# Optimization experiments

Hardware: AMD Instinct MI355X
Metric: run time of the kernel (lower is better)

## Reference

```python
import jax, jax.numpy as jnp
import numpy as np

INV_SCALE = 16.0  # 2 ** 4
DROPOUT_P = 0.2


def setup_inputs() -> dict:
    key = jax.random.key(0)
    ks = jax.random.split(key, 8)
    Nq, Nk, D = 8192, 8192, 32
    return {
        "x1": jax.random.normal(ks[0], (Nq, D), jnp.float32),
        "x2": jax.random.normal(ks[1], (Nk, D), jnp.float32),
        "wq_w": jax.random.normal(ks[2], (4, D), jnp.float32) * 0.1,
        "wq_b": jax.random.normal(ks[3], (4,), jnp.float32) * 0.1,
        "wk_w": jax.random.normal(ks[4], (4, D), jnp.float32) * 0.1,
        "wk_b": jax.random.normal(ks[5], (4,), jnp.float32) * 0.1,
        "wv_w": jax.random.normal(ks[6], (8, D), jnp.float32) * 0.1,
        "wv_b": jax.random.normal(ks[7], (8,), jnp.float32) * 0.1,
    }


def reference(x1, x2, wq_w, wq_b, wk_w, wk_b, wv_w, wv_b):
    # Linear projections (torch Linear: x @ W.T + b)
    q = x1 @ wq_w.T + wq_b          # [Nq, 4]
    k = x2 @ wk_w.T + wk_b          # [Nk, 4]
    v = x2 @ wv_w.T + wv_b          # [Nk, 8]
    scores = (q @ k.T) / INV_SCALE  # [Nq, Nk]
    probs = jax.nn.softmax(scores, axis=-1)
    # Inverted dropout with a fixed key (deterministic reference)
    keep = jax.random.bernoulli(jax.random.key(42), 1.0 - DROPOUT_P, probs.shape)
    dropped = jnp.where(keep, probs / (1.0 - DROPOUT_P), 0.0)
    return dropped @ v              # [Nq, 8]
```

## Files before the change

kernel.cpp:

```cpp
#include <hip/hip_runtime.h>
#include <stdint.h>

#define NQ 8192
#define NK 8192
#define DIN 32

#define BT 256
#define RPW 4
#define ROWS_PER_BLOCK 16
#define CHUNK 512

#define KEEP_BITS 3435974144u
#define QSCALE 0.0901684060119172f

__device__ __forceinline__ uint32_t rotl(uint32_t v, int d) {
    return __builtin_amdgcn_alignbit(v, v, 32 - d);
}

__device__ __forceinline__ void round4(uint32_t x0[4], uint32_t x1[4], int d) {
#pragma unroll
    for (int j = 0; j < 4; ++j) {
        x0[j] += x1[j];
        x1[j] = rotl(x1[j], d);
        x1[j] ^= x0[j];
    }
}

__device__ __forceinline__ void inject4(uint32_t x0[4], uint32_t x1[4],
                                        uint32_t c0, uint32_t c1) {
#pragma unroll
    for (int j = 0; j < 4; ++j) { x0[j] += c0; x1[j] += c1; }
}

__device__ __forceinline__ void threefry4(uint32_t idx0, uint32_t bits[4]) {
    const uint32_t ks1 = 42u;
    const uint32_t ks2 = 0x1BD11BDAu ^ 42u;
    uint32_t x0[4], x1[4];
#pragma unroll
    for (int j = 0; j < 4; ++j) {
        x0[j] = 0u;
        x1[j] = idx0 + (uint32_t)j * (uint32_t)NK + ks1;
    }
    round4(x0, x1, 13); round4(x0, x1, 15); round4(x0, x1, 26); round4(x0, x1, 6);
    inject4(x0, x1, ks1, ks2 + 1u);
    round4(x0, x1, 17); round4(x0, x1, 29); round4(x0, x1, 16); round4(x0, x1, 24);
    inject4(x0, x1, ks2, 0u + 2u);
    round4(x0, x1, 13); round4(x0, x1, 15); round4(x0, x1, 26); round4(x0, x1, 6);
    inject4(x0, x1, 0u, ks1 + 3u);
    round4(x0, x1, 17); round4(x0, x1, 29); round4(x0, x1, 16); round4(x0, x1, 24);
    inject4(x0, x1, ks1, ks2 + 4u);
    round4(x0, x1, 13); round4(x0, x1, 15); round4(x0, x1, 26); round4(x0, x1, 6);
#pragma unroll
    for (int j = 0; j < 4; ++j) bits[j] = (x0[j] + ks2) ^ (x1[j] + 0u + 5u);
}

__device__ __forceinline__ float fexp2(float x) {
#if __has_builtin(__builtin_amdgcn_exp2f)
    return __builtin_amdgcn_exp2f(x);
#else
    return __expf(0.6931471805599453f * x);
#endif
}

__global__ void proj_kernel(const float* __restrict__ x,
                            const float* __restrict__ w,
                            const float* __restrict__ b,
                            float* __restrict__ out, int dout) {
    __shared__ __align__(16) float ws[8 * DIN];
    __shared__ float bs[8];
    const int tid = threadIdx.x;
    if (tid < dout * DIN) ws[tid] = w[tid];
    if (tid < dout) bs[tid] = b[tid];
    __syncthreads();

    const int row = blockIdx.x * BT + tid;
    const float4* xr = reinterpret_cast<const float4*>(x + (size_t)row * DIN);
    float4 xv[8];
#pragma unroll
    for (int i = 0; i < 8; ++i) xv[i] = xr[i];

    for (int c = 0; c < dout; ++c) {
        float s = bs[c];
#pragma unroll
        for (int i = 0; i < 8; ++i) {
            const float4 wv = *reinterpret_cast<const float4*>(&ws[c * DIN + i * 4]);
            s += xv[i].x * wv.x + xv[i].y * wv.y + xv[i].z * wv.z + xv[i].w * wv.w;
        }
        out[(size_t)row * dout + c] = s;
    }
}

__global__ __launch_bounds__(BT) void attn_kernel(
    const float* __restrict__ q,
    const float* __restrict__ k,
    const float* __restrict__ v,
    float* __restrict__ partial,
    int ksplit) {
    __shared__ float4 lds_k[CHUNK];
    __shared__ float4 lds_va[CHUNK];
    __shared__ float4 lds_vb[CHUNK];

    const int tid = threadIdx.x;
    const int lane = tid & 63;
    const int wave = tid >> 6;
    const int split = blockIdx.y;
    const int qbase = blockIdx.x * ROWS_PER_BLOCK + wave * RPW;
    const int klen = NK / ksplit;
    const int kstart = split * klen;

    float4 qs[RPW];
#pragma unroll
    for (int r = 0; r < RPW; ++r) {
        float4 t = *reinterpret_cast<const float4*>(q + (size_t)(qbase + r) * 4);
        qs[r] = make_float4(t.x * QSCALE, t.y * QSCALE, t.z * QSCALE, t.w * QSCALE);
    }

    float4 accA[RPW], accB[RPW];
    float den[RPW];
#pragma unroll
    for (int r = 0; r < RPW; ++r) {
        accA[r] = make_float4(0.f, 0.f, 0.f, 0.f);
        accB[r] = make_float4(0.f, 0.f, 0.f, 0.f);
        den[r] = 0.f;
    }

    const float4* ksrc = reinterpret_cast<const float4*>(k);
    const float4* vsrc = reinterpret_cast<const float4*>(v);

    for (int base = kstart; base < kstart + klen; base += CHUNK) {
        __syncthreads();
#pragma unroll
        for (int i = tid; i < CHUNK; i += BT) {
            lds_k[i]  = ksrc[base + i];
            lds_va[i] = vsrc[2 * (base + i)];
            lds_vb[i] = vsrc[2 * (base + i) + 1];
        }
        __syncthreads();

        for (int kk = lane; kk < CHUNK; kk += 64) {
            const float4 kv = lds_k[kk];
            const float4 va = lds_va[kk];
            const float4 vb = lds_vb[kk];
            const uint32_t idx0 =
                (uint32_t)qbase * (uint32_t)NK + (uint32_t)(base + kk);

            uint32_t bits[RPW];
            threefry4(idx0, bits);

            float e[RPW];
#pragma unroll
            for (int r = 0; r < RPW; ++r) {
                const float s = qs[r].x * kv.x + qs[r].y * kv.y +
                                qs[r].z * kv.z + qs[r].w * kv.w;
                e[r] = fexp2(s);
            }
#pragma unroll
            for (int r = 0; r < RPW; ++r) {
                const float w = (bits[r] < KEEP_BITS) ? e[r] : 0.0f;
                den[r] += e[r];
                accA[r].x += w * va.x; accA[r].y += w * va.y;
                accA[r].z += w * va.z; accA[r].w += w * va.w;
                accB[r].x += w * vb.x; accB[r].y += w * vb.y;
                accB[r].z += w * vb.z; accB[r].w += w * vb.w;
            }
        }
    }

#pragma unroll
    for (int r = 0; r < RPW; ++r) {
        float n0 = accA[r].x, n1 = accA[r].y, n2 = accA[r].z, n3 = accA[r].w;
        float n4 = accB[r].x, n5 = accB[r].y, n6 = accB[r].z, n7 = accB[r].w;
        float dd = den[r];
#pragma unroll
        for (int off = 32; off >= 1; off >>= 1) {
            n0 += __shfl_xor(n0, off); n1 += __shfl_xor(n1, off);
            n2 += __shfl_xor(n2, off); n3 += __shfl_xor(n3, off);
            n4 += __shfl_xor(n4, off); n5 += __shfl_xor(n5, off);
            n6 += __shfl_xor(n6, off); n7 += __shfl_xor(n7, off);
            dd += __shfl_xor(dd, off);
        }
        if (lane == 0) {
            float* p = partial + ((size_t)split * NQ + (size_t)(qbase + r)) * 12;
            p[0] = n0; p[1] = n1; p[2] = n2; p[3] = n3;
            p[4] = n4; p[5] = n5; p[6] = n6; p[7] = n7;
            p[8] = dd;
        }
    }
}

__global__ void combine_kernel(const float* __restrict__ partial,
                               float* __restrict__ out, int ksplit) {
    const int row = blockIdx.x * 256 + threadIdx.x;
    float n[8] = {0.f, 0.f, 0.f, 0.f, 0.f, 0.f, 0.f, 0.f};
    float dd = 0.f;
    for (int s = 0; s < ksplit; ++s) {
        const float* p = partial + ((size_t)s * NQ + (size_t)row) * 12;
#pragma unroll
        for (int j = 0; j < 8; ++j) n[j] += p[j];
        dd += p[8];
    }
    const float inv = 1.0f / (0.8f * dd);
#pragma unroll
    for (int j = 0; j < 8; ++j) out[(size_t)row * 8 + j] = n[j] * inv;
}

extern "C" void kernel_launch(void* const* d_in, const int* in_sizes, int n_in,
                              void* d_out, int out_size, void* d_ws, size_t ws_size,
                              hipStream_t stream) {
    const float* x1   = (const float*)d_in[0];
    const float* x2   = (const float*)d_in[1];
    const float* wq_w = (const float*)d_in[2];
    const float* wq_b = (const float*)d_in[3];
    const float* wk_w = (const float*)d_in[4];
    const float* wk_b = (const float*)d_in[5];
    const float* wv_w = (const float*)d_in[6];
    const float* wv_b = (const float*)d_in[7];
    float* out = (float*)d_out;

    float* qws = (float*)d_ws;
    float* kws = qws + (size_t)NQ * 4;
    float* vws = kws + (size_t)NK * 4;
    float* pws = vws + (size_t)NK * 8;

    const size_t qkv_bytes = ((size_t)NQ * 4 + NK * 4 + NK * 8) * sizeof(float);
    int ksplit = 2;
    if (ws_size < qkv_bytes + (size_t)2 * NQ * 12 * sizeof(float)) ksplit = 1;

    proj_kernel<<<NQ / BT, BT, 0, stream>>>(x1, wq_w, wq_b, qws, 4);
    proj_kernel<<<NK / BT, BT, 0, stream>>>(x2, wk_w, wk_b, kws, 4);
    proj_kernel<<<NK / BT, BT, 0, stream>>>(x2, wv_w, wv_b, vws, 8);

    dim3 grid(NQ / ROWS_PER_BLOCK, ksplit);
    attn_kernel<<<grid, BT, 0, stream>>>(qws, kws, vws, pws, ksplit);

    combine_kernel<<<NQ / 256, 256, 0, stream>>>(pws, out, ksplit);
}
```

Baseline: 198.2 us.

## Drop LDS staging, read K/V directly, trim threefry ops, raise ksplit

Each wave now reads K and V straight from global memory (cache-resident, 384 KB total) instead of staging chunks in shared memory behind block barriers. The threefry rounds are restructured so the first round is folded into the initial state and key injections merge into the following round, cutting a few integer ops per sample. The split count over keys rises from 2 to 4, and launch bounds request 4 blocks per CU. The trade is more per-lane global/L2 loads and a larger partial buffer in exchange for no barriers, no LDS use and more parallelism.

```diff
diff --git a/kernel.cpp b/kernel.cpp
--- a/kernel.cpp
+++ b/kernel.cpp
@@ -8,50 +8,54 @@
 #define BT 256
 #define RPW 4
 #define ROWS_PER_BLOCK 16
-#define CHUNK 512
 
 #define KEEP_BITS 3435974144u
-#define QSCALE 0.0901684060119172f
+#define QSCALE 0.09016844005556021f
 
 __device__ __forceinline__ uint32_t rotl(uint32_t v, int d) {
     return __builtin_amdgcn_alignbit(v, v, 32 - d);
 }
 
-__device__ __forceinline__ void round4(uint32_t x0[4], uint32_t x1[4], int d) {
+__device__ __forceinline__ void tf_round(uint32_t x0[4], uint32_t x1[4], int d) {
 #pragma unroll
     for (int j = 0; j < 4; ++j) {
         x0[j] += x1[j];
-        x1[j] = rotl(x1[j], d);
-        x1[j] ^= x0[j];
-    }
-}
-
-__device__ __forceinline__ void inject4(uint32_t x0[4], uint32_t x1[4],
-                                        uint32_t c0, uint32_t c1) {
-#pragma unroll
-    for (int j = 0; j < 4; ++j) { x0[j] += c0; x1[j] += c1; }
-}
-
-__device__ __forceinline__ void threefry4(uint32_t idx0, uint32_t bits[4]) {
+        x1[j] = rotl(x1[j], d) ^ x0[j];
+    }
+}
+
+__device__ __forceinline__ void tf_round_inj(uint32_t x0[4], uint32_t x1[4],
+                                             uint32_t c0, uint32_t c1, int d) {
+#pragma unroll
+    for (int j = 0; j < 4; ++j) {
+        x1[j] += c1;
+        x0[j] = x0[j] + c0 + x1[j];
+        x1[j] = rotl(x1[j], d) ^ x0[j];
+    }
+}
+
+__device__ __forceinline__ void threefry4(uint32_t ctr, uint32_t bits[4]) {
     const uint32_t ks1 = 42u;
     const uint32_t ks2 = 0x1BD11BDAu ^ 42u;
     uint32_t x0[4], x1[4];
 #pragma unroll
     for (int j = 0; j < 4; ++j) {
-        x0[j] = 0u;
-        x1[j] = idx0 + (uint32_t)j * (uint32_t)NK + ks1;
-    }
-    round4(x0, x1, 13); round4(x0, x1, 15); round4(x0, x1, 26); round4(x0, x1, 6);
-    inject4(x0, x1, ks1, ks2 + 1u);
-    round4(x0, x1, 17); round4(x0, x1, 29); round4(x0, x1, 16); round4(x0, x1, 24);
-    inject4(x0, x1, ks2, 0u + 2u);
-    round4(x0, x1, 13); round4(x0, x1, 15); round4(x0, x1, 26); round4(x0, x1, 6);
-    inject4(x0, x1, 0u, ks1 + 3u);
-    round4(x0, x1, 17); round4(x0, x1, 29); round4(x0, x1, 16); round4(x0, x1, 24);
-    inject4(x0, x1, ks1, ks2 + 4u);
-    round4(x0, x1, 13); round4(x0, x1, 15); round4(x0, x1, 26); round4(x0, x1, 6);
-#pragma unroll
-    for (int j = 0; j < 4; ++j) bits[j] = (x0[j] + ks2) ^ (x1[j] + 0u + 5u);
+        const uint32_t t = ctr + ((uint32_t)j * (uint32_t)NK + ks1);
+        x0[j] = t;
+        x1[j] = rotl(t, 13) ^ t;
+    }
+    tf_round(x0, x1, 15); tf_round(x0, x1, 26); tf_round(x0, x1, 6);
+    tf_round_inj(x0, x1, ks1, ks2 + 1u, 17);
+    tf_round(x0, x1, 29); tf_round(x0, x1, 16); tf_round(x0, x1, 24);
+    tf_round_inj(x0, x1, ks2, 2u, 13);
+    tf_round(x0, x1, 15); tf_round(x0, x1, 26); tf_round(x0, x1, 6);
+    tf_round_inj(x0, x1, 0u, ks1 + 3u, 17);
+    tf_round(x0, x1, 29); tf_round(x0, x1, 16); tf_round(x0, x1, 24);
+    tf_round_inj(x0, x1, ks1, ks2 + 4u, 13);
+    tf_round(x0, x1, 15); tf_round(x0, x1, 26); tf_round(x0, x1, 6);
+#pragma unroll
+    for (int j = 0; j < 4; ++j)
+        bits[j] = (x0[j] + ks2) ^ (x1[j] + 5u);
 }
 
 __device__ __forceinline__ float fexp2(float x) {
@@ -90,16 +94,12 @@
     }
 }
 
-__global__ __launch_bounds__(BT) void attn_kernel(
+__global__ __launch_bounds__(BT, 4) void attn_kernel(
     const float* __restrict__ q,
     const float* __restrict__ k,
     const float* __restrict__ v,
     float* __restrict__ partial,
     int ksplit) {
-    __shared__ float4 lds_k[CHUNK];
-    __shared__ float4 lds_va[CHUNK];
-    __shared__ float4 lds_vb[CHUNK];
-
     const int tid = threadIdx.x;
     const int lane = tid & 63;
     const int wave = tid >> 6;
@@ -111,7 +111,7 @@
     float4 qs[RPW];
 #pragma unroll
     for (int r = 0; r < RPW; ++r) {
-        float4 t = *reinterpret_cast<const float4*>(q + (size_t)(qbase + r) * 4);
+        const float4 t = *reinterpret_cast<const float4*>(q + (size_t)(qbase + r) * 4);
         qs[r] = make_float4(t.x * QSCALE, t.y * QSCALE, t.z * QSCALE, t.w * QSCALE);
     }
 
@@ -124,45 +124,35 @@
         den[r] = 0.f;
     }
 
-    const float4* ksrc = reinterpret_cast<const float4*>(k);
-    const float4* vsrc = reinterpret_cast<const float4*>(v);
-
-    for (int base = kstart; base < kstart + klen; base += CHUNK) {
-        __syncthreads();
-#pragma unroll
-        for (int i = tid; i < CHUNK; i += BT) {
-            lds_k[i]  = ksrc[base + i];
-            lds_va[i] = vsrc[2 * (base + i)];
-            lds_vb[i] = vsrc[2 * (base + i) + 1];
-        }
-        __syncthreads();
-
-        for (int kk = lane; kk < CHUNK; kk += 64) {
-            const float4 kv = lds_k[kk];
-            const float4 va = lds_va[kk];
-            const float4 vb = lds_vb[kk];
-            const uint32_t idx0 =
-                (uint32_t)qbase * (uint32_t)NK + (uint32_t)(base + kk);
-
-            uint32_t bits[RPW];
-            threefry4(idx0, bits);
-
-            float e[RPW];
-#pragma unroll
-            for (int r = 0; r < RPW; ++r) {
-                const float s = qs[r].x * kv.x + qs[r].y * kv.y +
-                                qs[r].z * kv.z + qs[r].w * kv.w;
-                e[r] = fexp2(s);
-            }
-#pragma unroll
-            for (int r = 0; r < RPW; ++r) {
-                const float w = (bits[r] < KEEP_BITS) ? e[r] : 0.0f;
-                den[r] += e[r];
-                accA[r].x += w * va.x; accA[r].y += w * va.y;
-                accA[r].z += w * va.z; accA[r].w += w * va.w;
-                accB[r].x += w * vb.x; accB[r].y += w * vb.y;
-                accB[r].z += w * vb.z; accB[r].w += w * vb.w;
-            }
+    const float4* kp = reinterpret_cast<const float4*>(k) + (kstart + lane);
+    const float4* vp = reinterpret_cast<const float4*>(v) + 2 * (size_t)(kstart + lane);
+    uint32_t ctr = (uint32_t)qbase * (uint32_t)NK + (uint32_t)(kstart + lane);
+
+    const int iters = klen / 64;
+    for (int it = 0; it < iters; ++it) {
+        const float4 kv = kp[(size_t)it * 64];
+        const float4 va = vp[(size_t)it * 128];
+        const float4 vb = vp[(size_t)it * 128 + 1];
+
+        uint32_t bits[RPW];
+        threefry4(ctr, bits);
+        ctr += 64;
+
+        float e[RPW];
+#pragma unroll
+        for (int r = 0; r < RPW; ++r) {
+            const float s = qs[r].x * kv.x + qs[r].y * kv.y +
+                            qs[r].z * kv.z + qs[r].w * kv.w;
+            e[r] = fexp2(s);
+        }
+#pragma unroll
+        for (int r = 0; r < RPW; ++r) {
+            const float w = (bits[r] < KEEP_BITS) ? e[r] : 0.0f;
+            den[r] += e[r];
+            accA[r].x += w * va.x; accA[r].y += w * va.y;
+            accA[r].z += w * va.z; accA[r].w += w * va.w;
+            accB[r].x += w * vb.x; accB[r].y += w * vb.y;
+            accB[r].z += w * vb.z; accB[r].w += w * vb.w;
         }
     }
 
@@ -223,8 +213,9 @@
     float* pws = vws + (size_t)NK * 8;
 
     const size_t qkv_bytes = ((size_t)NQ * 4 + NK * 4 + NK * 8) * sizeof(float);
-    int ksplit = 2;
-    if (ws_size < qkv_bytes + (size_t)2 * NQ * 12 * sizeof(float)) ksplit = 1;
+    const size_t per_split = (size_t)NQ * 12 * sizeof(float);
+    int ksplit = 4;
+    while (ksplit > 1 && ws_size < qkv_bytes + (size_t)ksplit * per_split) ksplit >>= 1;
 
     proj_kernel<<<NQ / BT, BT, 0, stream>>>(x1, wq_w, wq_b, qws, 4);
     proj_kernel<<<NK / BT, BT, 0, stream>>>(x2, wk_w, wk_b, kws, 4);
```

Result: slower. 203.7 us (+2.8%).
